# Kernel optimization log

Hardware: AMD Instinct MI355X
Metric: run time of the kernel (lower is better)

The kernel has to match this reference:

```python
import jax, jax.numpy as jnp
import numpy as np

B, S, H, V, P = 16, 257, 768, 30522, 32  # batch, seq(incl CLS), hidden, vocab, tok_projection_dim


def setup_inputs() -> dict:
    key = jax.random.key(0)
    k1, k2, k3 = jax.random.split(key, 3)
    return {
        "hidden_states": jax.random.normal(k1, (B, S, H), jnp.float32),
        "logits": jax.random.normal(k2, (B, S, V), jnp.float32),
        "attention_mask": jnp.ones((B, S), jnp.float32),
        "W_tok": jax.random.normal(k3, (P, H), jnp.float32) * 0.02,
        "b_tok": jnp.zeros((P,), jnp.float32),
        "topk": 8,
    }


def reference(hidden_states, logits, attention_mask, W_tok, b_tok, topk):
    # strip [CLS] position, as in the torch forward
    hiddens = hidden_states[:, 1:, :]          # [B, S-1, H]
    mask = attention_mask[:, 1:]               # [B, S-1]
    lg = logits[:, 1:, :]                      # [B, S-1, V]

    full_router_repr = jnp.log1p(jax.nn.relu(lg)) * mask[:, :, None]   # [B, S-1, V]
    router_repr = jnp.max(full_router_repr, axis=1)                     # [B, V]

    expert_weights, expert_ids = jax.lax.top_k(full_router_repr, topk)  # [B, S-1, k]

    expert_repr = (jnp.einsum("bsh,ph->bsp", hiddens, W_tok) + b_tok) * mask[:, :, None]  # [B, S-1, P]

    b, s, v = full_router_repr.shape
    bi = jnp.arange(b)[:, None, None]
    si = jnp.arange(s)[None, :, None]
    router_mask = jnp.zeros_like(full_router_repr).at[bi, si, expert_ids].set(
        (expert_weights > 0.0).astype(full_router_repr.dtype)
    )                                                                   # [B, S-1, V]
    rm_seq = router_mask.sum(axis=1)                                    # [B, V]

    avg_cond_num_experts = rm_seq.sum(axis=1, keepdims=True).mean(axis=0, keepdims=True)  # [1, 1]
    avg_marg_num_experts = rm_seq.max(axis=0, keepdims=True).sum(axis=1, keepdims=True)   # [1, 1]

    router_softmax_sum = jax.nn.softmax(lg, axis=-1).sum(axis=1)        # [B, V]

    return (
        avg_cond_num_experts,
        avg_marg_num_experts,
        rm_seq,                # ret['router_mask']
        router_softmax_sum,    # ret['router_softmax_repr']
        mask,                  # ret['attention_mask']
        router_repr,
        expert_ids,
        expert_repr,
        expert_weights,
    )
```

## Files before the change

kernel.cpp:

```cpp
#include <hip/hip_runtime.h>
#include <hip/hip_bf16.h>
#include <float.h>

#define BB 16
#define SS 257
#define SP 256
#define HH 768
#define VV 30522
#define NF2 15261
#define PP 32
#define KK 8
#define CAP 2048

__global__ __launch_bounds__(256) void rowstats_kernel(
    const float* __restrict__ logits, const float* __restrict__ amask,
    float* __restrict__ invZ, float* __restrict__ o_rm,
    float* __restrict__ o_mask, float* __restrict__ o_ids,
    float* __restrict__ o_w)
{
  const int tid = threadIdx.x;
  const int row = blockIdx.x;
  const int b = row >> 8, s = row & 255;
  const float* lp = logits + (size_t)(b * SS + s + 1) * VV;
  const float mval = amask[b * SS + s + 1];
  const bool mz = (mval != 0.0f);

  __shared__ float cv[CAP];
  __shared__ int   ci[CAP];
  __shared__ float red[4];
  __shared__ int   cnt;
  if (tid == 0) cnt = 0;
  __syncthreads();

  const float2* lp2 = (const float2*)lp;
  const float T = 3.0f;
  float z0 = 0.0f, z1 = 0.0f, z2 = 0.0f, z3 = 0.0f;
  for (int k = 0; k < 56; k += 4) {
    float2 x0 = lp2[tid + 256 * (k + 0)];
    float2 x1 = lp2[tid + 256 * (k + 1)];
    float2 x2 = lp2[tid + 256 * (k + 2)];
    float2 x3 = lp2[tid + 256 * (k + 3)];
    z0 += __expf(x0.x) + __expf(x0.y);
    z1 += __expf(x1.x) + __expf(x1.y);
    z2 += __expf(x2.x) + __expf(x2.y);
    z3 += __expf(x3.x) + __expf(x3.y);
    if (mz) {
      if (x0.x > T) { int p = atomicAdd(&cnt, 1); if (p < CAP) { cv[p] = x0.x; ci[p] = 2 * (tid + 256 * (k + 0)); } }
      if (x0.y > T) { int p = atomicAdd(&cnt, 1); if (p < CAP) { cv[p] = x0.y; ci[p] = 2 * (tid + 256 * (k + 0)) + 1; } }
      if (x1.x > T) { int p = atomicAdd(&cnt, 1); if (p < CAP) { cv[p] = x1.x; ci[p] = 2 * (tid + 256 * (k + 1)); } }
      if (x1.y > T) { int p = atomicAdd(&cnt, 1); if (p < CAP) { cv[p] = x1.y; ci[p] = 2 * (tid + 256 * (k + 1)) + 1; } }
      if (x2.x > T) { int p = atomicAdd(&cnt, 1); if (p < CAP) { cv[p] = x2.x; ci[p] = 2 * (tid + 256 * (k + 2)); } }
      if (x2.y > T) { int p = atomicAdd(&cnt, 1); if (p < CAP) { cv[p] = x2.y; ci[p] = 2 * (tid + 256 * (k + 2)) + 1; } }
      if (x3.x > T) { int p = atomicAdd(&cnt, 1); if (p < CAP) { cv[p] = x3.x; ci[p] = 2 * (tid + 256 * (k + 3)); } }
      if (x3.y > T) { int p = atomicAdd(&cnt, 1); if (p < CAP) { cv[p] = x3.y; ci[p] = 2 * (tid + 256 * (k + 3)) + 1; } }
    }
  }
  for (int k = 56; k < 60; ++k) {
    int c = tid + 256 * k;
    if (c < NF2) {
      float2 x = lp2[c];
      z0 += __expf(x.x) + __expf(x.y);
      if (mz) {
        if (x.x > T) { int p = atomicAdd(&cnt, 1); if (p < CAP) { cv[p] = x.x; ci[p] = 2 * c; } }
        if (x.y > T) { int p = atomicAdd(&cnt, 1); if (p < CAP) { cv[p] = x.y; ci[p] = 2 * c + 1; } }
      }
    }
  }
  float zsum = (z0 + z1) + (z2 + z3);
  #pragma unroll
  for (int off = 32; off; off >>= 1) zsum += __shfl_xor(zsum, off, 64);
  if ((tid & 63) == 0) red[tid >> 6] = zsum;
  __syncthreads();
  if (tid == 0) invZ[row] = 1.0f / ((red[0] + red[1]) + (red[2] + red[3]));

  int n = cnt;
  if (n < KK || n > CAP) {
    float lv[KK]; int li[KK];
    #pragma unroll
    for (int j = 0; j < KK; ++j) { lv[j] = -1.0f; li[j] = 0; }
    for (int c = tid; c < NF2; c += 256) {
      float2 x = lp2[c];
      float v0 = mz ? fmaxf(x.x, 0.0f) : 0.0f;
      float v1 = mz ? fmaxf(x.y, 0.0f) : 0.0f;
      if (v0 > lv[KK - 1]) {
        #pragma unroll
        for (int j = KK - 1; j >= 1; --j) {
          bool a = lv[j - 1] < v0;
          bool q = lv[j] < v0;
          lv[j] = a ? lv[j - 1] : (q ? v0 : lv[j]);
          li[j] = a ? li[j - 1] : (q ? (2 * c) : li[j]);
        }
        if (lv[0] < v0) { lv[0] = v0; li[0] = 2 * c; }
      }
      if (v1 > lv[KK - 1]) {
        #pragma unroll
        for (int j = KK - 1; j >= 1; --j) {
          bool a = lv[j - 1] < v1;
          bool q = lv[j] < v1;
          lv[j] = a ? lv[j - 1] : (q ? v1 : lv[j]);
          li[j] = a ? li[j - 1] : (q ? (2 * c + 1) : li[j]);
        }
        if (lv[0] < v1) { lv[0] = v1; li[0] = 2 * c + 1; }
      }
    }
    #pragma unroll
    for (int j = 0; j < KK; ++j) { cv[tid * KK + j] = lv[j]; ci[tid * KK + j] = li[j]; }
    n = CAP;
    __syncthreads();
  }

  if (tid < 64) {
    #pragma unroll 1
    for (int kk = 0; kk < KK; ++kk) {
      float mv = -FLT_MAX; int mi = 0x7fffffff; int ms = -1;
      for (int j = tid; j < n; j += 64) {
        float v = cv[j]; int ix = ci[j];
        if (v > mv || (v == mv && ix < mi)) { mv = v; mi = ix; ms = j; }
      }
      #pragma unroll
      for (int off = 32; off; off >>= 1) {
        float ov = __shfl_xor(mv, off, 64);
        int   oi = __shfl_xor(mi, off, 64);
        int   os = __shfl_xor(ms, off, 64);
        if (ov > mv || (ov == mv && oi < mi)) { mv = ov; mi = oi; ms = os; }
      }
      if (tid == 0) cv[ms] = -FLT_MAX;
      if (tid == kk) {
        float w = mval * log1pf(fmaxf(mv, 0.0f));
        o_w[(size_t)row * KK + kk] = w;
        o_ids[(size_t)row * KK + kk] = (float)mi;
        if (w > 0.0f) atomicAdd(&o_rm[(size_t)b * VV + mi], 1.0f);
      }
    }
  }
  if (tid == 0) o_mask[row] = mval;
}

__global__ __launch_bounds__(256) void colstats_kernel(
    const float* __restrict__ logits, const float* __restrict__ amask,
    const float* __restrict__ invZ,
    float* __restrict__ o_rss, float* __restrict__ o_rrepr)
{
  const int b = blockIdx.y;
  const int tid = threadIdx.x;
  const int c = blockIdx.x * 256 + tid;
  __shared__ float zi[SP];
  __shared__ float mm[SP];
  zi[tid] = invZ[b * SP + tid];
  mm[tid] = amask[b * SS + 1 + tid];
  __syncthreads();
  if (c >= NF2) return;
  const float2* base = (const float2*)(logits + (size_t)(b * SS + 1) * VV) + c;
  float a0 = 0, a1 = 0, b0 = 0, b1 = 0, e0 = 0, e1 = 0, f0 = 0, f1 = 0;
  float g0 = 0, g1 = 0, h0 = 0, h1 = 0, i0 = 0, i1 = 0, j0 = 0, j1 = 0;
  #pragma unroll 2
  for (int s = 0; s < 64; ++s) {
    float2 x0 = base[(size_t)(s)       * NF2];
    float2 x1 = base[(size_t)(s +  64) * NF2];
    float2 x2 = base[(size_t)(s + 128) * NF2];
    float2 x3 = base[(size_t)(s + 192) * NF2];
    a0 = fmaf(__expf(x0.x), zi[s      ], a0);  a1 = fmaf(__expf(x0.y), zi[s      ], a1);
    b0 = fmaf(__expf(x1.x), zi[s +  64], b0);  b1 = fmaf(__expf(x1.y), zi[s +  64], b1);
    e0 = fmaf(__expf(x2.x), zi[s + 128], e0);  e1 = fmaf(__expf(x2.y), zi[s + 128], e1);
    f0 = fmaf(__expf(x3.x), zi[s + 192], f0);  f1 = fmaf(__expf(x3.y), zi[s + 192], f1);
    g0 = fmaxf(g0, mm[s      ] != 0.f ? x0.x : 0.f); g1 = fmaxf(g1, mm[s      ] != 0.f ? x0.y : 0.f);
    h0 = fmaxf(h0, mm[s +  64] != 0.f ? x1.x : 0.f); h1 = fmaxf(h1, mm[s +  64] != 0.f ? x1.y : 0.f);
    i0 = fmaxf(i0, mm[s + 128] != 0.f ? x2.x : 0.f); i1 = fmaxf(i1, mm[s + 128] != 0.f ? x2.y : 0.f);
    j0 = fmaxf(j0, mm[s + 192] != 0.f ? x3.x : 0.f); j1 = fmaxf(j1, mm[s + 192] != 0.f ? x3.y : 0.f);
  }
  float sa = (a0 + b0) + (e0 + f0);
  float sb = (a1 + b1) + (e1 + f1);
  float ma = fmaxf(fmaxf(g0, h0), fmaxf(i0, j0));
  float mb = fmaxf(fmaxf(g1, h1), fmaxf(i1, j1));
  size_t o = (size_t)b * VV + 2 * (size_t)c;
  *(float2*)(o_rss + o)   = make_float2(sa, sb);
  *(float2*)(o_rrepr + o) = make_float2(log1pf(ma), log1pf(mb));
}

__global__ __launch_bounds__(256) void transw_kernel(
    const float* __restrict__ W, float* __restrict__ Wt)
{
  int i = blockIdx.x * 256 + threadIdx.x;
  if (i < PP * HH) {
    int p = i / HH, k = i % HH;
    Wt[k * PP + p] = W[i];
  }
}

__global__ __launch_bounds__(256) void expertk_kernel(
    const float* __restrict__ hs, const float* __restrict__ amask,
    const float* __restrict__ Wt, const float* __restrict__ btok,
    float* __restrict__ o_er)
{
  const int row = blockIdx.x;
  const int b = row >> 8, s = row & 255;
  const float* hp = hs + (size_t)(b * SS + s + 1) * HH;
  __shared__ float h[HH];
  __shared__ float psum[8][PP];
  for (int i = threadIdx.x; i < HH; i += 256) h[i] = hp[i];
  __syncthreads();
  const int p = threadIdx.x & 31, g = threadIdx.x >> 5;
  float acc = 0.0f;
  #pragma unroll 8
  for (int k = g * 96; k < g * 96 + 96; ++k) acc = fmaf(h[k], Wt[k * PP + p], acc);
  psum[g][p] = acc;
  __syncthreads();
  if (threadIdx.x < PP) {
    float r = 0.0f;
    #pragma unroll
    for (int g2 = 0; g2 < 8; ++g2) r += psum[g2][threadIdx.x];
    float mval = amask[b * SS + s + 1];
    o_er[(size_t)row * PP + threadIdx.x] = (r + btok[threadIdx.x]) * mval;
  }
}

__global__ __launch_bounds__(256) void reducerm_kernel(
    const float* __restrict__ rm, float* __restrict__ out01)
{
  int v = blockIdx.x * 256 + threadIdx.x;
  float sm = 0.0f, mx = 0.0f;
  if (v < VV) {
    #pragma unroll
    for (int b = 0; b < BB; ++b) {
      float r = rm[(size_t)b * VV + v];
      sm += r; mx = fmaxf(mx, r);
    }
  }
  __shared__ float rs[256], rx[256];
  rs[threadIdx.x] = sm; rx[threadIdx.x] = mx;
  __syncthreads();
  #pragma unroll
  for (int st = 128; st > 0; st >>= 1) {
    if (threadIdx.x < st) {
      rs[threadIdx.x] += rs[threadIdx.x + st];
      rx[threadIdx.x] += rx[threadIdx.x + st];
    }
    __syncthreads();
  }
  if (threadIdx.x == 0) {
    atomicAdd(&out01[0], rs[0] * (1.0f / BB));
    atomicAdd(&out01[1], rx[0]);
  }
}

extern "C" void kernel_launch(void* const* d_in, const int* in_sizes, int n_in,
                              void* d_out, int out_size, void* d_ws, size_t ws_size,
                              hipStream_t stream) {
  const float* hs     = (const float*)d_in[0];
  const float* logits = (const float*)d_in[1];
  const float* amask  = (const float*)d_in[2];
  const float* W      = (const float*)d_in[3];
  const float* btok   = (const float*)d_in[4];

  float* out    = (float*)d_out;
  float* o_cond = out;
  float* o_rm   = out + 2;
  float* o_rss  = o_rm + (size_t)BB * VV;
  float* o_mask = o_rss + (size_t)BB * VV;
  float* o_rrepr= o_mask + (size_t)BB * SP;
  float* o_ids  = o_rrepr + (size_t)BB * VV;
  float* o_er   = o_ids + (size_t)BB * SP * KK;
  float* o_w    = o_er + (size_t)BB * SP * PP;

  float* wsf  = (float*)d_ws;
  float* invZ = wsf;
  float* Wt   = wsf + 4096;

  hipMemsetAsync(out, 0, (2 + (size_t)BB * VV) * sizeof(float), stream);

  rowstats_kernel<<<BB * SP, 256, 0, stream>>>(logits, amask, invZ, o_rm, o_mask, o_ids, o_w);
  colstats_kernel<<<dim3((NF2 + 255) / 256, BB), 256, 0, stream>>>(logits, amask, invZ, o_rss, o_rrepr);
  transw_kernel<<<(PP * HH + 255) / 256, 256, 0, stream>>>(W, Wt);
  expertk_kernel<<<BB * SP, 256, 0, stream>>>(hs, amask, Wt, btok, o_er);
  reducerm_kernel<<<(VV + 255) / 256, 256, 0, stream>>>(o_rm, o_cond);
}
```

Baseline: 787.2 us.

## Chunk row/col stats by batch for cache reuse; tile expert projection over rows

The rowstats and colstats passes are interleaved in batch chunks so each chunk's logits can remain in the last-level cache between the two reads, instead of streaming the full logits tensor twice from HBM. The expert projection kernel now processes 8 rows per block and stages W in shared memory, cutting redundant weight loads. This costs more kernel launches with smaller grids, which can lower occupancy per launch.

```diff
diff --git a/kernel.cpp b/kernel.cpp
--- a/kernel.cpp
+++ b/kernel.cpp
@@ -11,15 +11,16 @@
 #define PP 32
 #define KK 8
 #define CAP 2048
+#define CHB 4
 
 __global__ __launch_bounds__(256) void rowstats_kernel(
     const float* __restrict__ logits, const float* __restrict__ amask,
     float* __restrict__ invZ, float* __restrict__ o_rm,
     float* __restrict__ o_mask, float* __restrict__ o_ids,
-    float* __restrict__ o_w)
+    float* __restrict__ o_w, int b0)
 {
   const int tid = threadIdx.x;
-  const int row = blockIdx.x;
+  const int row = b0 * SP + blockIdx.x;
   const int b = row >> 8, s = row & 255;
   const float* lp = logits + (size_t)(b * SS + s + 1) * VV;
   const float mval = amask[b * SS + s + 1];
@@ -139,9 +140,9 @@
 __global__ __launch_bounds__(256) void colstats_kernel(
     const float* __restrict__ logits, const float* __restrict__ amask,
     const float* __restrict__ invZ,
-    float* __restrict__ o_rss, float* __restrict__ o_rrepr)
-{
-  const int b = blockIdx.y;
+    float* __restrict__ o_rss, float* __restrict__ o_rrepr, int b0)
+{
+  const int b = b0 + blockIdx.y;
   const int tid = threadIdx.x;
   const int c = blockIdx.x * 256 + tid;
   __shared__ float zi[SP];
@@ -151,7 +152,7 @@
   __syncthreads();
   if (c >= NF2) return;
   const float2* base = (const float2*)(logits + (size_t)(b * SS + 1) * VV) + c;
-  float a0 = 0, a1 = 0, b0 = 0, b1 = 0, e0 = 0, e1 = 0, f0 = 0, f1 = 0;
+  float a0 = 0, a1 = 0, b0v = 0, b1v = 0, e0 = 0, e1 = 0, f0 = 0, f1 = 0;
   float g0 = 0, g1 = 0, h0 = 0, h1 = 0, i0 = 0, i1 = 0, j0 = 0, j1 = 0;
   #pragma unroll 2
   for (int s = 0; s < 64; ++s) {
@@ -159,17 +160,17 @@
     float2 x1 = base[(size_t)(s +  64) * NF2];
     float2 x2 = base[(size_t)(s + 128) * NF2];
     float2 x3 = base[(size_t)(s + 192) * NF2];
-    a0 = fmaf(__expf(x0.x), zi[s      ], a0);  a1 = fmaf(__expf(x0.y), zi[s      ], a1);
-    b0 = fmaf(__expf(x1.x), zi[s +  64], b0);  b1 = fmaf(__expf(x1.y), zi[s +  64], b1);
-    e0 = fmaf(__expf(x2.x), zi[s + 128], e0);  e1 = fmaf(__expf(x2.y), zi[s + 128], e1);
-    f0 = fmaf(__expf(x3.x), zi[s + 192], f0);  f1 = fmaf(__expf(x3.y), zi[s + 192], f1);
+    a0  = fmaf(__expf(x0.x), zi[s      ], a0 );  a1  = fmaf(__expf(x0.y), zi[s      ], a1 );
+    b0v = fmaf(__expf(x1.x), zi[s +  64], b0v);  b1v = fmaf(__expf(x1.y), zi[s +  64], b1v);
+    e0  = fmaf(__expf(x2.x), zi[s + 128], e0 );  e1  = fmaf(__expf(x2.y), zi[s + 128], e1 );
+    f0  = fmaf(__expf(x3.x), zi[s + 192], f0 );  f1  = fmaf(__expf(x3.y), zi[s + 192], f1 );
     g0 = fmaxf(g0, mm[s      ] != 0.f ? x0.x : 0.f); g1 = fmaxf(g1, mm[s      ] != 0.f ? x0.y : 0.f);
     h0 = fmaxf(h0, mm[s +  64] != 0.f ? x1.x : 0.f); h1 = fmaxf(h1, mm[s +  64] != 0.f ? x1.y : 0.f);
     i0 = fmaxf(i0, mm[s + 128] != 0.f ? x2.x : 0.f); i1 = fmaxf(i1, mm[s + 128] != 0.f ? x2.y : 0.f);
     j0 = fmaxf(j0, mm[s + 192] != 0.f ? x3.x : 0.f); j1 = fmaxf(j1, mm[s + 192] != 0.f ? x3.y : 0.f);
   }
-  float sa = (a0 + b0) + (e0 + f0);
-  float sb = (a1 + b1) + (e1 + f1);
+  float sa = (a0 + b0v) + (e0 + f0);
+  float sb = (a1 + b1v) + (e1 + f1);
   float ma = fmaxf(fmaxf(g0, h0), fmaxf(i0, j0));
   float mb = fmaxf(fmaxf(g1, h1), fmaxf(i1, j1));
   size_t o = (size_t)b * VV + 2 * (size_t)c;
@@ -192,26 +193,29 @@
     const float* __restrict__ Wt, const float* __restrict__ btok,
     float* __restrict__ o_er)
 {
-  const int row = blockIdx.x;
-  const int b = row >> 8, s = row & 255;
-  const float* hp = hs + (size_t)(b * SS + s + 1) * HH;
-  __shared__ float h[HH];
-  __shared__ float psum[8][PP];
-  for (int i = threadIdx.x; i < HH; i += 256) h[i] = hp[i];
-  __syncthreads();
-  const int p = threadIdx.x & 31, g = threadIdx.x >> 5;
+  const int tid = threadIdx.x;
+  const int row0 = blockIdx.x * 8;
+  const int b = row0 >> 8, s0 = row0 & 255;
+  const float* hp = hs + (size_t)(b * SS + s0 + 1) * HH;
+  __shared__ float h[8 * HH];
+  __shared__ float wt[64 * PP];
+  const float4* hp4 = (const float4*)hp;
+  float4* h4 = (float4*)h;
+  #pragma unroll
+  for (int i = 0; i < 6; ++i) h4[tid + 256 * i] = hp4[tid + 256 * i];
+  const int p = tid & 31, rg = tid >> 5;
   float acc = 0.0f;
-  #pragma unroll 8
-  for (int k = g * 96; k < g * 96 + 96; ++k) acc = fmaf(h[k], Wt[k * PP + p], acc);
-  psum[g][p] = acc;
-  __syncthreads();
-  if (threadIdx.x < PP) {
-    float r = 0.0f;
-    #pragma unroll
-    for (int g2 = 0; g2 < 8; ++g2) r += psum[g2][threadIdx.x];
-    float mval = amask[b * SS + s + 1];
-    o_er[(size_t)row * PP + threadIdx.x] = (r + btok[threadIdx.x]) * mval;
-  }
+  for (int k0 = 0; k0 < HH; k0 += 64) {
+    __syncthreads();
+    #pragma unroll
+    for (int i = 0; i < 8; ++i) wt[tid + 256 * i] = Wt[k0 * PP + tid + 256 * i];
+    __syncthreads();
+    #pragma unroll
+    for (int k = 0; k < 64; ++k)
+      acc = fmaf(h[rg * HH + k0 + k], wt[k * PP + p], acc);
+  }
+  float mval = amask[b * SS + s0 + rg + 1];
+  o_er[(size_t)(row0 + rg) * PP + p] = (acc + btok[p]) * mval;
 }
 
 __global__ __launch_bounds__(256) void reducerm_kernel(
@@ -268,9 +272,13 @@
 
   hipMemsetAsync(out, 0, (2 + (size_t)BB * VV) * sizeof(float), stream);
 
-  rowstats_kernel<<<BB * SP, 256, 0, stream>>>(logits, amask, invZ, o_rm, o_mask, o_ids, o_w);
-  colstats_kernel<<<dim3((NF2 + 255) / 256, BB), 256, 0, stream>>>(logits, amask, invZ, o_rss, o_rrepr);
   transw_kernel<<<(PP * HH + 255) / 256, 256, 0, stream>>>(W, Wt);
-  expertk_kernel<<<BB * SP, 256, 0, stream>>>(hs, amask, Wt, btok, o_er);
+
+  for (int b0 = 0; b0 < BB; b0 += CHB) {
+    rowstats_kernel<<<CHB * SP, 256, 0, stream>>>(logits, amask, invZ, o_rm, o_mask, o_ids, o_w, b0);
+    colstats_kernel<<<dim3((NF2 + 255) / 256, CHB), 256, 0, stream>>>(logits, amask, invZ, o_rss, o_rrepr, b0);
+  }
+
+  expertk_kernel<<<(BB * SP) / 8, 256, 0, stream>>>(hs, amask, Wt, btok, o_er);
   reducerm_kernel<<<(VV + 255) / 256, 256, 0, stream>>>(o_rm, o_cond);
 }
```

Result: slower. 819.8 us (+4.1%).
